# Kernel optimization log

Measured on AMD Instinct MI355X. Metric: run time of the kernel, lower is better.

## Reference

```python
import jax, jax.numpy as jnp
import numpy as np

COMMITMENT_COST = 0.25


def _mlp(x, Ws, bs):
    # Linear layers with ReLU between hidden layers, linear output (rlpyt-style MlpModel).
    n = len(Ws)
    for i in range(n):
        x = x @ Ws[i] + bs[i]
        if i < n - 1:
            x = jax.nn.relu(x)
    return x


def setup_inputs() -> dict:
    key = jax.random.key(0)
    ks = jax.random.split(key, 16)
    B, D_in, H1, H2, D_code, K = 16384, 1024, 2048, 1024, 256, 1024

    def lin(kw, kb, fan_in, fan_out):
        lim = 1.0 / np.sqrt(fan_in)
        W = jax.random.uniform(kw, (fan_in, fan_out), jnp.float32, -lim, lim)
        b = jax.random.uniform(kb, (fan_out,), jnp.float32, -lim, lim)
        return W, b

    enc_W1, enc_b1 = lin(ks[0], ks[1], D_in, H1)
    enc_W2, enc_b2 = lin(ks[2], ks[3], H1, H2)
    enc_W3, enc_b3 = lin(ks[4], ks[5], H2, D_code)
    dec_W1, dec_b1 = lin(ks[6], ks[7], D_code, H2)
    dec_W2, dec_b2 = lin(ks[8], ks[9], H2, H1)
    dec_W3, dec_b3 = lin(ks[10], ks[11], H1, D_in)
    codebook = jax.random.uniform(ks[12], (K, D_code), jnp.float32, -1.0 / K, 1.0 / K)
    x = jax.random.normal(ks[13], (B, D_in), jnp.float32)
    return {
        "x": x,
        "enc_W1": enc_W1, "enc_b1": enc_b1,
        "enc_W2": enc_W2, "enc_b2": enc_b2,
        "enc_W3": enc_W3, "enc_b3": enc_b3,
        "codebook": codebook,
        "dec_W1": dec_W1, "dec_b1": dec_b1,
        "dec_W2": dec_W2, "dec_b2": dec_b2,
        "dec_W3": dec_W3, "dec_b3": dec_b3,
    }


def reference(x, enc_W1, enc_b1, enc_W2, enc_b2, enc_W3, enc_b3, codebook,
              dec_W1, dec_b1, dec_W2, dec_b2, dec_W3, dec_b3):
    # Encoder MLP -> z: [B, D_code]
    z = _mlp(x, [enc_W1, enc_W2, enc_W3], [enc_b1, enc_b2, enc_b3])
    # Squared L2 distances z vs codebook: [B, K]
    distances = (jnp.sum(z * z, axis=1, keepdims=True)
                 + jnp.sum(codebook * codebook, axis=1)
                 - 2.0 * jnp.einsum('bd,kd->bk', z, codebook))
    indices = jnp.argmin(distances, axis=1)  # [B]
    # one-hot scatter + matmul in the original == direct gather
    quantized = codebook[indices]            # [B, D_code]
    # training-mode losses
    e_latent_loss = jnp.mean((jax.lax.stop_gradient(quantized) - z) ** 2)
    q_latent_loss = jnp.mean((quantized - jax.lax.stop_gradient(z)) ** 2)
    loss = q_latent_loss + COMMITMENT_COST * e_latent_loss
    # straight-through estimator
    quantized_st = z + jax.lax.stop_gradient(quantized - z)
    reconstructed = _mlp(quantized_st, [dec_W1, dec_W2, dec_W3], [dec_b1, dec_b2, dec_b3])
    return reconstructed, quantized_st, loss, indices[:, None]
```

## Files before the change

### kernel.cpp

```cpp
#include <hip/hip_runtime.h>
#include <hip/hip_bf16.h>
#include <stdint.h>


#define BDIM  16384
#define DIN   1024
#define DH1   2048
#define DH2   1024
#define DCODE 256
#define KCODE 1024

typedef __hip_bfloat16 bf16;
typedef __attribute__((ext_vector_type(8))) short short8;
typedef __attribute__((ext_vector_type(4))) float f32x4;

__device__ __forceinline__ void gload16(const void* g, void* l)
{
    __builtin_amdgcn_global_load_lds(
        (const __attribute__((address_space(1))) unsigned int*)g,
        (__attribute__((address_space(3))) unsigned int*)l, 16, 0, 0);
}

__device__ __forceinline__ void split3(float f, ushort* h, ushort* m, ushort* l)
{
    bf16 bh = __float2bfloat16(f);
    float r1 = f - __bfloat162float(bh);
    bf16 bm = __float2bfloat16(r1);
    float r2 = r1 - __bfloat162float(bm);
    bf16 bl = __float2bfloat16(r2);
    *h = *(ushort*)&bh; *m = *(ushort*)&bm; *l = *(ushort*)&bl;
}

template<int RELU, int OUTK>
__global__ __launch_bounds__(512, 2)
void gemms(const ushort* __restrict__ Apl, const ushort* __restrict__ Bpl,
           const float* __restrict__ bias, void* __restrict__ C,
           void* __restrict__ C2,
           int M, int N, int K, size_t PA, size_t PB, size_t PC)
{
    __shared__ __align__(16) short As[3][128][32];
    __shared__ __align__(16) short Bs[3][128][32];
    const int tid  = threadIdx.x;
    const int lane = tid & 63;
    const int wave = tid >> 6;
    const int wm = (wave >> 1) << 5;
    const int wn = (wave & 1) << 6;
    const int fr = lane & 15, fq = lane >> 4;
    const int row0 = blockIdx.y << 7, col0 = blockIdx.x << 7;

    const int srow = (wave << 4) + (lane >> 2);
    const int sslot = lane & 3;
    const int skg = (sslot ^ ((srow >> 1) & 3)) << 3;

    const ushort* AgT = Apl + (size_t)(row0 + srow) * K + skg;
    const ushort* BgT = Bpl + (size_t)(col0 + srow) * K + skg;

    f32x4  acc[2][4];
    double dacc[2][4][4];
    #pragma unroll
    for (int i = 0; i < 2; ++i)
        #pragma unroll
        for (int j = 0; j < 4; ++j) {
            acc[i][j] = (f32x4)0.0f;
            #pragma unroll
            for (int r = 0; r < 4; ++r) dacc[i][j][r] = 0.0;
        }

    const int nsteps = K >> 5;
    for (int s = 0; s < nsteps; ++s) {
        const int kb = s << 5;
        #pragma unroll
        for (int p = 0; p < 3; ++p) {
            gload16(AgT + (size_t)p * PA + kb, &As[p][wave << 4][0]);
            gload16(BgT + (size_t)p * PB + kb, &Bs[p][wave << 4][0]);
        }
        __syncthreads();

        short8 bh[4], bm[4], bl[4];
        #pragma unroll
        for (int j = 0; j < 4; ++j) {
            const int bn = wn + (j << 4) + fr;
            const int bs = (fq ^ ((bn >> 1) & 3)) << 3;
            bh[j] = *(const short8*)&Bs[0][bn][bs];
            bm[j] = *(const short8*)&Bs[1][bn][bs];
            bl[j] = *(const short8*)&Bs[2][bn][bs];
        }
        #pragma unroll
        for (int i = 0; i < 2; ++i) {
            const int an = wm + (i << 4) + fr;
            const int asl = (fq ^ ((an >> 1) & 3)) << 3;
            short8 ah = *(const short8*)&As[0][an][asl];
            short8 am = *(const short8*)&As[1][an][asl];
            short8 al = *(const short8*)&As[2][an][asl];
            #pragma unroll
            for (int j = 0; j < 4; ++j) {
                acc[i][j] = __builtin_amdgcn_mfma_f32_16x16x32_bf16(ah, bh[j], acc[i][j], 0, 0, 0);
                acc[i][j] = __builtin_amdgcn_mfma_f32_16x16x32_bf16(ah, bm[j], acc[i][j], 0, 0, 0);
                acc[i][j] = __builtin_amdgcn_mfma_f32_16x16x32_bf16(am, bh[j], acc[i][j], 0, 0, 0);
                acc[i][j] = __builtin_amdgcn_mfma_f32_16x16x32_bf16(ah, bl[j], acc[i][j], 0, 0, 0);
                acc[i][j] = __builtin_amdgcn_mfma_f32_16x16x32_bf16(al, bh[j], acc[i][j], 0, 0, 0);
                acc[i][j] = __builtin_amdgcn_mfma_f32_16x16x32_bf16(am, bm[j], acc[i][j], 0, 0, 0);
            }
        }

        if (s & 1) {
            #pragma unroll
            for (int i = 0; i < 2; ++i)
                #pragma unroll
                for (int j = 0; j < 4; ++j) {
                    #pragma unroll
                    for (int r = 0; r < 4; ++r) dacc[i][j][r] += (double)acc[i][j][r];
                    acc[i][j] = (f32x4)0.0f;
                }
        }
        __syncthreads();
    }
    #pragma unroll
    for (int i = 0; i < 2; ++i)
        #pragma unroll
        for (int j = 0; j < 4; ++j)
            #pragma unroll
            for (int r = 0; r < 4; ++r) dacc[i][j][r] += (double)acc[i][j][r];

    #pragma unroll
    for (int j = 0; j < 4; ++j) {
        const int n = col0 + wn + (j << 4) + fr;
        const double bv = (double)bias[n];
        #pragma unroll
        for (int i = 0; i < 2; ++i) {
            const int mb = row0 + wm + (i << 4) + (fq << 2);
            #pragma unroll
            for (int r = 0; r < 4; ++r) {
                double v = dacc[i][j][r] + bv;
                if (RELU) v = v > 0.0 ? v : 0.0;
                const size_t o = (size_t)(mb + r) * N + n;
                if (OUTK == 2 || OUTK == 3) ((double*)C)[o] = v;
                if (OUTK == 0 || OUTK == 3) {
                    ushort h, m, l;
                    split3((float)v, &h, &m, &l);
                    ushort* Cp = (ushort*)((OUTK == 0) ? C : C2);
                    Cp[o] = h; Cp[PC + o] = m; Cp[2 * PC + o] = l;
                }
            }
        }
    }
}

__global__ __launch_bounds__(512, 2)
void distm(const ushort* __restrict__ Zpl, const ushort* __restrict__ Cpl,
           const double* __restrict__ c2, double* __restrict__ psc,
           int* __restrict__ pix)
{
    __shared__ __align__(16) short As[3][128][40];
    __shared__ __align__(16) short Bs[3][128][40];
    const int tid  = threadIdx.x;
    const int lane = tid & 63;
    const int wave = tid >> 6;
    const int wm = (wave >> 1) << 5;
    const int wn = (wave & 1) << 6;
    const int fr = lane & 15, fq = lane >> 4;
    const int row0 = blockIdx.y << 7, col0 = blockIdx.x << 7;
    const int sr = tid >> 2, sc = (tid & 3) << 3;
    const size_t PZ = (size_t)BDIM * DCODE;
    const size_t PC = (size_t)KCODE * DCODE;

    const ushort* Ag = Zpl + (size_t)(row0 + sr) * DCODE + sc;
    const ushort* Bg = Cpl + (size_t)(col0 + sr) * DCODE + sc;

    f32x4  acc[2][4];
    double dacc[2][4][4];
    #pragma unroll
    for (int i = 0; i < 2; ++i)
        #pragma unroll
        for (int j = 0; j < 4; ++j) {
            acc[i][j] = (f32x4)0.0f;
            #pragma unroll
            for (int r = 0; r < 4; ++r) dacc[i][j][r] = 0.0;
        }

    short8 sa[3], sb[3];
    #pragma unroll
    for (int p = 0; p < 3; ++p) {
        sa[p] = *(const short8*)(Ag + (size_t)p * PZ);
        sb[p] = *(const short8*)(Bg + (size_t)p * PC);
    }

    const int nsteps = DCODE >> 5;
    for (int s = 0; s < nsteps; ++s) {
        __syncthreads();
        #pragma unroll
        for (int p = 0; p < 3; ++p) {
            *(short8*)&As[p][sr][sc] = sa[p];
            *(short8*)&Bs[p][sr][sc] = sb[p];
        }
        __syncthreads();
        if (s + 1 < nsteps) {
            const int kb = (s + 1) << 5;
            #pragma unroll
            for (int p = 0; p < 3; ++p) {
                sa[p] = *(const short8*)(Ag + (size_t)p * PZ + kb);
                sb[p] = *(const short8*)(Bg + (size_t)p * PC + kb);
            }
        }

        short8 bh[4], bm[4], bl[4];
        #pragma unroll
        for (int j = 0; j < 4; ++j) {
            const int bn = wn + (j << 4) + fr;
            bh[j] = *(const short8*)&Bs[0][bn][fq << 3];
            bm[j] = *(const short8*)&Bs[1][bn][fq << 3];
            bl[j] = *(const short8*)&Bs[2][bn][fq << 3];
        }
        #pragma unroll
        for (int i = 0; i < 2; ++i) {
            const int an = wm + (i << 4) + fr;
            short8 ah = *(const short8*)&As[0][an][fq << 3];
            short8 am = *(const short8*)&As[1][an][fq << 3];
            short8 al = *(const short8*)&As[2][an][fq << 3];
            #pragma unroll
            for (int j = 0; j < 4; ++j) {
                acc[i][j] = __builtin_amdgcn_mfma_f32_16x16x32_bf16(ah, bh[j], acc[i][j], 0, 0, 0);
                acc[i][j] = __builtin_amdgcn_mfma_f32_16x16x32_bf16(ah, bm[j], acc[i][j], 0, 0, 0);
                acc[i][j] = __builtin_amdgcn_mfma_f32_16x16x32_bf16(am, bh[j], acc[i][j], 0, 0, 0);
                acc[i][j] = __builtin_amdgcn_mfma_f32_16x16x32_bf16(ah, bl[j], acc[i][j], 0, 0, 0);
                acc[i][j] = __builtin_amdgcn_mfma_f32_16x16x32_bf16(al, bh[j], acc[i][j], 0, 0, 0);
                acc[i][j] = __builtin_amdgcn_mfma_f32_16x16x32_bf16(am, bm[j], acc[i][j], 0, 0, 0);
            }
        }

        if (s & 1) {
            #pragma unroll
            for (int i = 0; i < 2; ++i)
                #pragma unroll
                for (int j = 0; j < 4; ++j) {
                    #pragma unroll
                    for (int r = 0; r < 4; ++r) dacc[i][j][r] += (double)acc[i][j][r];
                    acc[i][j] = (f32x4)0.0f;
                }
        }
    }
    #pragma unroll
    for (int i = 0; i < 2; ++i)
        #pragma unroll
        for (int j = 0; j < 4; ++j)
            #pragma unroll
            for (int r = 0; r < 4; ++r) dacc[i][j][r] += (double)acc[i][j][r];

    __syncthreads();
    double* scb = (double*)&As[0][0][0];
    int*    sib = (int*)(scb + 256);

    #pragma unroll
    for (int i = 0; i < 2; ++i) {
        #pragma unroll
        for (int r = 0; r < 4; ++r) {
            double bs = 1e300; int bi = 0;
            #pragma unroll
            for (int j = 0; j < 4; ++j) {
                const int n = col0 + wn + (j << 4) + fr;
                const double s = c2[n] - 2.0 * dacc[i][j][r];
                if (s < bs) { bs = s; bi = n; }
            }
            #pragma unroll
            for (int msk = 1; msk < 16; msk <<= 1) {
                double os = __shfl_xor(bs, msk, 64);
                int    oi = __shfl_xor(bi, msk, 64);
                if (os < bs || (os == bs && oi < bi)) { bs = os; bi = oi; }
            }
            if (fr == 0) {
                const int lr = wm + (i << 4) + (fq << 2) + r;
                scb[lr * 2 + (wave & 1)] = bs;
                sib[lr * 2 + (wave & 1)] = bi;
            }
        }
    }
    __syncthreads();
    if (tid < 128) {
        double s0 = scb[tid * 2], s1 = scb[tid * 2 + 1];
        int    i0 = sib[tid * 2], i1 = sib[tid * 2 + 1];
        const bool t1 = (s1 < s0) || (s1 == s0 && i1 < i0);
        const size_t o = (size_t)(row0 + tid) * (KCODE / 128) + blockIdx.x;
        psc[o] = t1 ? s1 : s0;
        pix[o] = t1 ? i1 : i0;
    }
}

__global__ __launch_bounds__(256)
void reduce8(const double* __restrict__ psc, const int* __restrict__ pix,
             int* __restrict__ idx_out)
{
    const int row = blockIdx.x * 256 + threadIdx.x;
    const double* ps = psc + (size_t)row * (KCODE / 128);
    const int*    pi = pix + (size_t)row * (KCODE / 128);
    double m = ps[0]; int mi = pi[0];
    #pragma unroll
    for (int t = 1; t < KCODE / 128; ++t) {
        double s = ps[t]; int c = pi[t];
        if (s < m || (s == m && c < mi)) { m = s; mi = c; }
    }
    idx_out[row] = mi;
}

template<int RELU, int OUTBF>
__global__ __launch_bounds__(256)
void gemmb2(const ushort* __restrict__ A, const ushort* __restrict__ Bt,
            const float* __restrict__ bias, void* __restrict__ C,
            int M, int N, int K)
{
    __shared__ __align__(16) short As[128][32];
    __shared__ __align__(16) short Bs[128][32];
    const int tid  = threadIdx.x;
    const int lane = tid & 63;
    const int wave = tid >> 6;
    const int wm = (wave >> 1) << 6, wn = (wave & 1) << 6;
    const int fr = lane & 15;
    const int fq = lane >> 4;
    const int row0 = blockIdx.y << 7, col0 = blockIdx.x << 7;

    const int sr0 = (wave << 5) + (lane >> 2);
    const int sslot = lane & 3;
    const int kg0 = (sslot ^ ((sr0 >> 1) & 3)) << 3;
    const int sr1 = sr0 + 16;
    const int kg1 = (sslot ^ ((sr1 >> 1) & 3)) << 3;

    const ushort* Ag0 = A  + (size_t)(row0 + sr0) * K + kg0;
    const ushort* Ag1 = A  + (size_t)(row0 + sr1) * K + kg1;
    const ushort* Bg0 = Bt + (size_t)(col0 + sr0) * K + kg0;
    const ushort* Bg1 = Bt + (size_t)(col0 + sr1) * K + kg1;

    f32x4 acc[4][4];
    #pragma unroll
    for (int i = 0; i < 4; ++i)
        #pragma unroll
        for (int j = 0; j < 4; ++j) acc[i][j] = (f32x4)0.0f;

    for (int kb = 0; kb < K; kb += 32) {
        gload16(Ag0 + kb, &As[(wave << 5)][0]);
        gload16(Ag1 + kb, &As[(wave << 5) + 16][0]);
        gload16(Bg0 + kb, &Bs[(wave << 5)][0]);
        gload16(Bg1 + kb, &Bs[(wave << 5) + 16][0]);
        __syncthreads();

        short8 af[4], bf[4];
        #pragma unroll
        for (int i = 0; i < 4; ++i) {
            const int an = wm + (i << 4) + fr;
            af[i] = *(const short8*)&As[an][(fq ^ ((an >> 1) & 3)) << 3];
        }
        #pragma unroll
        for (int j = 0; j < 4; ++j) {
            const int bn = wn + (j << 4) + fr;
            bf[j] = *(const short8*)&Bs[bn][(fq ^ ((bn >> 1) & 3)) << 3];
        }
        #pragma unroll
        for (int i = 0; i < 4; ++i)
            #pragma unroll
            for (int j = 0; j < 4; ++j)
                acc[i][j] = __builtin_amdgcn_mfma_f32_16x16x32_bf16(
                                af[i], bf[j], acc[i][j], 0, 0, 0);
        __syncthreads();
    }

    #pragma unroll
    for (int j = 0; j < 4; ++j) {
        const int n = col0 + wn + (j << 4) + fr;
        const float bv = bias[n];
        #pragma unroll
        for (int i = 0; i < 4; ++i) {
            const int mb = row0 + wm + (i << 4) + (fq << 2);
            #pragma unroll
            for (int r = 0; r < 4; ++r) {
                float v = acc[i][j][r] + bv;
                if (RELU) v = fmaxf(v, 0.0f);
                size_t o = (size_t)(mb + r) * N + n;
                if (OUTBF) ((bf16*)C)[o]  = __float2bfloat16(v);
                else       ((float*)C)[o] = v;
            }
        }
    }
}

__global__ __launch_bounds__(256)
void wtrans(const float* __restrict__ W, ushort* __restrict__ Wt, int K, int N)
{
    __shared__ float tile[64][65];
    const int tid = threadIdx.x;
    const int kb = blockIdx.y << 6, nb = blockIdx.x << 6;
    const int r = tid >> 4, c4 = (tid & 15) << 2;
    #pragma unroll
    for (int s = 0; s < 4; ++s) {
        float4 v = *(const float4*)(W + (size_t)(kb + r + (s << 4)) * N + nb + c4);
        tile[r + (s << 4)][c4 + 0] = v.x; tile[r + (s << 4)][c4 + 1] = v.y;
        tile[r + (s << 4)][c4 + 2] = v.z; tile[r + (s << 4)][c4 + 3] = v.w;
    }
    __syncthreads();
    #pragma unroll
    for (int s = 0; s < 4; ++s) {
        const int n = r + (s << 4);
        ushort u[4];
        #pragma unroll
        for (int l = 0; l < 4; ++l) {
            bf16 h = __float2bfloat16(tile[c4 + l][n]);
            u[l] = *(ushort*)&h;
        }
        *(ushort4*)(Wt + (size_t)(nb + n) * K + kb + c4) = make_ushort4(u[0], u[1], u[2], u[3]);
    }
}

__global__ __launch_bounds__(256)
void wsplit(const float* __restrict__ W, ushort* __restrict__ Wt, int K, int N)
{
    __shared__ float tile[64][65];
    const int tid = threadIdx.x;
    const int kb = blockIdx.y << 6, nb = blockIdx.x << 6;
    const int r = tid >> 4, c4 = (tid & 15) << 2;
    const size_t NK = (size_t)N * K;
    #pragma unroll
    for (int s = 0; s < 4; ++s) {
        float4 v = *(const float4*)(W + (size_t)(kb + r + (s << 4)) * N + nb + c4);
        tile[r + (s << 4)][c4 + 0] = v.x; tile[r + (s << 4)][c4 + 1] = v.y;
        tile[r + (s << 4)][c4 + 2] = v.z; tile[r + (s << 4)][c4 + 3] = v.w;
    }
    __syncthreads();
    #pragma unroll
    for (int s = 0; s < 4; ++s) {
        const int n = r + (s << 4);
        ushort h[4], m[4], l[4];
        #pragma unroll
        for (int e = 0; e < 4; ++e) split3(tile[c4 + e][n], &h[e], &m[e], &l[e]);
        const size_t o = (size_t)(nb + n) * K + kb + c4;
        *(ushort4*)(Wt + o)          = make_ushort4(h[0], h[1], h[2], h[3]);
        *(ushort4*)(Wt + NK + o)     = make_ushort4(m[0], m[1], m[2], m[3]);
        *(ushort4*)(Wt + 2 * NK + o) = make_ushort4(l[0], l[1], l[2], l[3]);
    }
}

__global__ __launch_bounds__(256)
void xsplit(const float* __restrict__ X, ushort* __restrict__ Xp, size_t P)
{
    const size_t i = ((size_t)blockIdx.x * 256 + threadIdx.x) << 2;
    float4 v = *(const float4*)(X + i);
    ushort h[4], m[4], l[4];
    split3(v.x, &h[0], &m[0], &l[0]);
    split3(v.y, &h[1], &m[1], &l[1]);
    split3(v.z, &h[2], &m[2], &l[2]);
    split3(v.w, &h[3], &m[3], &l[3]);
    *(ushort4*)(Xp + i)         = make_ushort4(h[0], h[1], h[2], h[3]);
    *(ushort4*)(Xp + P + i)     = make_ushort4(m[0], m[1], m[2], m[3]);
    *(ushort4*)(Xp + 2 * P + i) = make_ushort4(l[0], l[1], l[2], l[3]);
}

__global__ __launch_bounds__(64)
void c2_k(const float* __restrict__ cb, double* __restrict__ c2)
{
    int code = blockIdx.x, l = threadIdx.x;
    float4 v = *(const float4*)(cb + (size_t)code * DCODE + (l << 2));
    double s = (double)v.x * v.x + (double)v.y * v.y
             + (double)v.z * v.z + (double)v.w * v.w;
    #pragma unroll
    for (int off = 32; off; off >>= 1) s += __shfl_down(s, off, 64);
    if (l == 0) c2[code] = s;
}

__global__ __launch_bounds__(256)
void gather_k(const int* __restrict__ idx_in, const float* __restrict__ cb,
              const double* __restrict__ z, ushort* __restrict__ qstb,
              float* __restrict__ out_qst, float* __restrict__ out_idx,
              double* __restrict__ psum)
{
    const int tid  = threadIdx.x;
    const int row  = (blockIdx.x << 2) + (tid >> 6);
    const int lane = tid & 63;
    const int d    = lane << 2;
    const int idx  = idx_in[row];

    float4 qv = *(const float4*)(cb + (size_t)idx * DCODE + d);
    const double* zp = z + (size_t)row * DCODE + d;
    double2 z0 = *(const double2*)(zp);
    double2 z1 = *(const double2*)(zp + 2);

    double q[4] = {(double)qv.x, (double)qv.y, (double)qv.z, (double)qv.w};
    double zz[4] = {z0.x, z0.y, z1.x, z1.y};
    double qs[4];
    double s = 0.0;
    #pragma unroll
    for (int e = 0; e < 4; ++e) {
        double diff = q[e] - zz[e];
        qs[e] = zz[e] + diff;
        s += diff * diff;
    }
    *(float4*)(out_qst + (size_t)row * DCODE + d) =
        make_float4((float)qs[0], (float)qs[1], (float)qs[2], (float)qs[3]);
    ushort u[4];
    #pragma unroll
    for (int e = 0; e < 4; ++e) {
        bf16 h = __float2bfloat16((float)qs[e]);
        u[e] = *(ushort*)&h;
    }
    *(ushort4*)(qstb + (size_t)row * DCODE + d) = make_ushort4(u[0], u[1], u[2], u[3]);

    #pragma unroll
    for (int off = 32; off; off >>= 1) s += __shfl_down(s, off, 64);
    __shared__ double sred[4];
    if (lane == 0) {
        sred[tid >> 6] = s;
        out_idx[row] = (float)idx;
    }
    __syncthreads();
    if (tid == 0) psum[blockIdx.x] = sred[0] + sred[1] + sred[2] + sred[3];
}

__global__ __launch_bounds__(256)
void loss_k(const double* __restrict__ psum, float* __restrict__ out_loss)
{
    const int tid = threadIdx.x;
    double s = 0.0;
    for (int i = tid; i < BDIM / 4; i += 256) s += psum[i];
    #pragma unroll
    for (int off = 32; off; off >>= 1) s += __shfl_down(s, off, 64);
    __shared__ double sred[4];
    if ((tid & 63) == 0) sred[tid >> 6] = s;
    __syncthreads();
    if (tid == 0)
        out_loss[0] = (float)(1.25 * (sred[0] + sred[1] + sred[2] + sred[3]) / 4194304.0);
}

extern "C" void kernel_launch(void* const* d_in, const int* in_sizes, int n_in,
                              void* d_out, int out_size, void* d_ws, size_t ws_size,
                              hipStream_t stream)
{
    const float* x   = (const float*)d_in[0];
    const float* eW1 = (const float*)d_in[1];
    const float* eb1 = (const float*)d_in[2];
    const float* eW2 = (const float*)d_in[3];
    const float* eb2 = (const float*)d_in[4];
    const float* eW3 = (const float*)d_in[5];
    const float* eb3 = (const float*)d_in[6];
    const float* cbk = (const float*)d_in[7];
    const float* dW1 = (const float*)d_in[8];
    const float* db1 = (const float*)d_in[9];
    const float* dW2 = (const float*)d_in[10];
    const float* db2 = (const float*)d_in[11];
    const float* dW3 = (const float*)d_in[12];
    const float* db3 = (const float*)d_in[13];

    const size_t EPS1 = (size_t)3 * 2048 * 1024 * 2;
    const size_t EPS2 = (size_t)3 * 1024 * 2048 * 2;
    const size_t EPS3 = (size_t)3 * 256 * 1024 * 2;
    const size_t EPS  = EPS1 + EPS2 + EPS3;
    const size_t FIX_W1 = (size_t)1024 * 256 * 2;
    const size_t FIX_W2 = (size_t)2048 * 1024 * 2;
    const size_t FIX_W3 = (size_t)1024 * 2048 * 2;
    const size_t ZB   = (size_t)BDIM * DCODE * 8;
    const size_t ZPLB = (size_t)3 * BDIM * DCODE * 2;
    const size_t QSTB = (size_t)BDIM * DCODE * 2;
    const size_t IDXB = (size_t)BDIM * 4;
    const size_t NPT  = KCODE / 128;
    const size_t PSCB = (size_t)BDIM * NPT * 8;
    const size_t PIXB = (size_t)BDIM * NPT * 4;
    const size_t CBPB = (size_t)3 * KCODE * DCODE * 2;
    const size_t PSUM = (size_t)(BDIM / 4) * 8;

    const size_t PERSIST = FIX_W1 + FIX_W2 + FIX_W3 + ZB + ZPLB + QSTB + IDXB
                         + PSCB + PIXB + CBPB + PSUM + 8192 + 256;

    int R = BDIM;
    while (R > 256 && PERSIST + EPS + (size_t)R * 24576 > ws_size) R >>= 1;
    const int nch = BDIM / R;

    char* ws = (char*)d_ws;
    size_t off = 0;
    ushort* eP1  = (ushort*)(ws + off); off += EPS1;
    ushort* eP2  = (ushort*)(ws + off); off += EPS2;
    ushort* eP3  = (ushort*)(ws + off); off += EPS3;
    ushort* xpl  = (ushort*)(ws + off); off += (size_t)R * 6144;
    ushort* h1pl = (ushort*)(ws + off); off += (size_t)R * 12288;
    ushort* h2pl = (ushort*)(ws + off); off += (size_t)R * 6144;
    ushort* dh1b = xpl;
    ushort* dh2b = h1pl;
    ushort* Wt1  = (ushort*)(ws + off); off += FIX_W1;
    ushort* Wt2  = (ushort*)(ws + off); off += FIX_W2;
    ushort* Wt3  = (ushort*)(ws + off); off += FIX_W3;
    double* zb   = (double*)(ws + off); off += ZB;
    ushort* zpl  = (ushort*)(ws + off); off += ZPLB;
    ushort* qstb = (ushort*)(ws + off); off += QSTB;
    int*    idxb = (int*)(ws + off);    off += IDXB;
    double* psc  = (double*)(ws + off); off += PSCB;
    int*    pix  = (int*)(ws + off);    off += PIXB;
    ushort* cbP  = (ushort*)(ws + off); off += CBPB;
    double* psum = (double*)(ws + off); off += PSUM;
    double* c2   = (double*)(ws + off); off += 8192;

    float* out      = (float*)d_out;
    float* out_rec  = out;
    float* out_qst  = out + (size_t)BDIM * DIN;
    float* out_loss = out_qst + (size_t)BDIM * DCODE;
    float* out_idx  = out_loss + 1;

    c2_k<<<KCODE, 64, 0, stream>>>(cbk, c2);
    wtrans<<<dim3(1024 / 64,  256 / 64), 256, 0, stream>>>(dW1, Wt1,  256, 1024);
    wtrans<<<dim3(2048 / 64, 1024 / 64), 256, 0, stream>>>(dW2, Wt2, 1024, 2048);
    wtrans<<<dim3(1024 / 64, 2048 / 64), 256, 0, stream>>>(dW3, Wt3, 2048, 1024);
    wsplit<<<dim3(2048 / 64, 1024 / 64), 256, 0, stream>>>(eW1, eP1, 1024, 2048);
    wsplit<<<dim3(1024 / 64, 2048 / 64), 256, 0, stream>>>(eW2, eP2, 2048, 1024);
    wsplit<<<dim3( 256 / 64, 1024 / 64), 256, 0, stream>>>(eW3, eP3, 1024,  256);
    xsplit<<<(KCODE * DCODE) / 1024, 256, 0, stream>>>(cbk, cbP, (size_t)KCODE * DCODE);

    for (int c = 0; c < nch; ++c) {
        const float* xc = x + (size_t)c * R * DIN;
        double* zb_c  = zb + (size_t)c * R * DCODE;
        ushort* zpl_c = zpl + (size_t)c * R * DCODE;
        xsplit<<<R, 256, 0, stream>>>(xc, xpl, (size_t)R * DIN);
        gemms<1, 0><<<dim3(DH1 / 128, R / 128), 512, 0, stream>>>(
            xpl, eP1, eb1, h1pl, nullptr, R, DH1, DIN,
            (size_t)R * DIN, (size_t)DH1 * DIN, (size_t)R * DH1);
        gemms<1, 0><<<dim3(DH2 / 128, R / 128), 512, 0, stream>>>(
            h1pl, eP2, eb2, h2pl, nullptr, R, DH2, DH1,
            (size_t)R * DH1, (size_t)DH2 * DH1, (size_t)R * DH2);
        gemms<0, 3><<<dim3(DCODE / 128, R / 128), 512, 0, stream>>>(
            h2pl, eP3, eb3, zb_c, zpl_c, R, DCODE, DH2,
            (size_t)R * DH2, (size_t)DCODE * DH2, (size_t)BDIM * DCODE);
    }

    distm<<<dim3(KCODE / 128, BDIM / 128), 512, 0, stream>>>(zpl, cbP, c2, psc, pix);
    reduce8<<<BDIM / 256, 256, 0, stream>>>(psc, pix, idxb);

    gather_k<<<BDIM / 4, 256, 0, stream>>>(idxb, cbk, zb, qstb, out_qst, out_idx, psum);

    for (int c = 0; c < nch; ++c) {
        const ushort* qst_c = qstb + (size_t)c * R * DCODE;
        float* rec_c = out_rec + (size_t)c * R * DIN;
        gemmb2<1, 1><<<dim3(DH2 / 128, R / 128), 256, 0, stream>>>(qst_c, Wt1, db1, dh1b, R, DH2, DCODE);
        gemmb2<1, 1><<<dim3(DH1 / 128, R / 128), 256, 0, stream>>>(dh1b, Wt2, db2, dh2b, R, DH1, DH2);
        gemmb2<0, 0><<<dim3(DIN / 128, R / 128), 256, 0, stream>>>(dh2b, Wt3, db3, rec_c, R, DIN, DH1);
    }

    loss_k<<<1, 256, 0, stream>>>(psum, out_loss);
}
```

Baseline: 1.721 ms.

## Double-buffer LDS tiles in both GEMM kernels to overlap loads with MFMA

Both GEMM kernels get a second LDS buffer. The tile for step s+1 is now issued with global_load_lds before computing on step s, and a partial s_waitcnt vmcnt lets the current tile's loads finish while the next ones stay in flight. This hides global memory latency behind the MFMA work instead of stalling at a barrier every step. In exchange, LDS use doubles (the 3-plane kernel goes to 48KB per block at 2 blocks/CU), which may reduce occupancy. Correctness also depends on the hand-written vmcnt values matching the number of loads the compiler emits.

```diff
diff --git a/kernel.cpp b/kernel.cpp
--- a/kernel.cpp
+++ b/kernel.cpp
@@ -38,8 +38,8 @@
            void* __restrict__ C2,
            int M, int N, int K, size_t PA, size_t PB, size_t PC)
 {
-    __shared__ __align__(16) short As[3][128][32];
-    __shared__ __align__(16) short Bs[3][128][32];
+    __shared__ __align__(16) short As[2][3][128][32];
+    __shared__ __align__(16) short Bs[2][3][128][32];
     const int tid  = threadIdx.x;
     const int lane = tid & 63;
     const int wave = tid >> 6;
@@ -66,32 +66,43 @@
             for (int r = 0; r < 4; ++r) dacc[i][j][r] = 0.0;
         }
 
+    auto stage = [&](int b, int kb) {
+        #pragma unroll
+        for (int p = 0; p < 3; ++p) {
+            gload16(AgT + (size_t)p * PA + kb, &As[b][p][wave << 4][0]);
+            gload16(BgT + (size_t)p * PB + kb, &Bs[b][p][wave << 4][0]);
+        }
+    };
+
+    stage(0, 0);
     const int nsteps = K >> 5;
     for (int s = 0; s < nsteps; ++s) {
-        const int kb = s << 5;
-        #pragma unroll
-        for (int p = 0; p < 3; ++p) {
-            gload16(AgT + (size_t)p * PA + kb, &As[p][wave << 4][0]);
-            gload16(BgT + (size_t)p * PB + kb, &Bs[p][wave << 4][0]);
-        }
-        __syncthreads();
+        const int b = s & 1;
+        if (s + 1 < nsteps) {
+            stage(b ^ 1, (s + 1) << 5);
+            asm volatile("s_waitcnt vmcnt(6)" ::: "memory");
+        } else {
+            asm volatile("s_waitcnt vmcnt(0)" ::: "memory");
+        }
+        __builtin_amdgcn_s_barrier();
+        __builtin_amdgcn_sched_barrier(0);
 
         short8 bh[4], bm[4], bl[4];
         #pragma unroll
         for (int j = 0; j < 4; ++j) {
             const int bn = wn + (j << 4) + fr;
-            const int bs = (fq ^ ((bn >> 1) & 3)) << 3;
-            bh[j] = *(const short8*)&Bs[0][bn][bs];
-            bm[j] = *(const short8*)&Bs[1][bn][bs];
-            bl[j] = *(const short8*)&Bs[2][bn][bs];
+            const int bsl = (fq ^ ((bn >> 1) & 3)) << 3;
+            bh[j] = *(const short8*)&Bs[b][0][bn][bsl];
+            bm[j] = *(const short8*)&Bs[b][1][bn][bsl];
+            bl[j] = *(const short8*)&Bs[b][2][bn][bsl];
         }
         #pragma unroll
         for (int i = 0; i < 2; ++i) {
             const int an = wm + (i << 4) + fr;
             const int asl = (fq ^ ((an >> 1) & 3)) << 3;
-            short8 ah = *(const short8*)&As[0][an][asl];
-            short8 am = *(const short8*)&As[1][an][asl];
-            short8 al = *(const short8*)&As[2][an][asl];
+            short8 ah = *(const short8*)&As[b][0][an][asl];
+            short8 am = *(const short8*)&As[b][1][an][asl];
+            short8 al = *(const short8*)&As[b][2][an][asl];
             #pragma unroll
             for (int j = 0; j < 4; ++j) {
                 acc[i][j] = __builtin_amdgcn_mfma_f32_16x16x32_bf16(ah, bh[j], acc[i][j], 0, 0, 0);
@@ -113,7 +124,8 @@
                     acc[i][j] = (f32x4)0.0f;
                 }
         }
-        __syncthreads();
+        __builtin_amdgcn_sched_barrier(0);
+        __builtin_amdgcn_s_barrier();
     }
     #pragma unroll
     for (int i = 0; i < 2; ++i)
@@ -307,8 +319,8 @@
             const float* __restrict__ bias, void* __restrict__ C,
             int M, int N, int K)
 {
-    __shared__ __align__(16) short As[128][32];
-    __shared__ __align__(16) short Bs[128][32];
+    __shared__ __align__(16) short As[2][128][32];
+    __shared__ __align__(16) short Bs[2][128][32];
     const int tid  = threadIdx.x;
     const int lane = tid & 63;
     const int wave = tid >> 6;
@@ -334,23 +346,36 @@
         #pragma unroll
         for (int j = 0; j < 4; ++j) acc[i][j] = (f32x4)0.0f;
 
-    for (int kb = 0; kb < K; kb += 32) {
-        gload16(Ag0 + kb, &As[(wave << 5)][0]);
-        gload16(Ag1 + kb, &As[(wave << 5) + 16][0]);
-        gload16(Bg0 + kb, &Bs[(wave << 5)][0]);
-        gload16(Bg1 + kb, &Bs[(wave << 5) + 16][0]);
-        __syncthreads();
+    auto stage = [&](int b, int kb) {
+        gload16(Ag0 + kb, &As[b][wave << 5][0]);
+        gload16(Ag1 + kb, &As[b][(wave << 5) + 16][0]);
+        gload16(Bg0 + kb, &Bs[b][wave << 5][0]);
+        gload16(Bg1 + kb, &Bs[b][(wave << 5) + 16][0]);
+    };
+
+    stage(0, 0);
+    const int nsteps = K >> 5;
+    for (int s = 0; s < nsteps; ++s) {
+        const int b = s & 1;
+        if (s + 1 < nsteps) {
+            stage(b ^ 1, (s + 1) << 5);
+            asm volatile("s_waitcnt vmcnt(4)" ::: "memory");
+        } else {
+            asm volatile("s_waitcnt vmcnt(0)" ::: "memory");
+        }
+        __builtin_amdgcn_s_barrier();
+        __builtin_amdgcn_sched_barrier(0);
 
         short8 af[4], bf[4];
         #pragma unroll
         for (int i = 0; i < 4; ++i) {
             const int an = wm + (i << 4) + fr;
-            af[i] = *(const short8*)&As[an][(fq ^ ((an >> 1) & 3)) << 3];
+            af[i] = *(const short8*)&As[b][an][(fq ^ ((an >> 1) & 3)) << 3];
         }
         #pragma unroll
         for (int j = 0; j < 4; ++j) {
             const int bn = wn + (j << 4) + fr;
-            bf[j] = *(const short8*)&Bs[bn][(fq ^ ((bn >> 1) & 3)) << 3];
+            bf[j] = *(const short8*)&Bs[b][bn][(fq ^ ((bn >> 1) & 3)) << 3];
         }
         #pragma unroll
         for (int i = 0; i < 4; ++i)
@@ -358,7 +383,9 @@
             for (int j = 0; j < 4; ++j)
                 acc[i][j] = __builtin_amdgcn_mfma_f32_16x16x32_bf16(
                                 af[i], bf[j], acc[i][j], 0, 0, 0);
-        __syncthreads();
+
+        __builtin_amdgcn_sched_barrier(0);
+        __builtin_amdgcn_s_barrier();
     }
 
     #pragma unroll
```

Measured after the change: 1.588 ms. 7.7% less time.
